# Kernel optimization log

Hardware: AMD Instinct MI355X
Metric: run time of the kernel (lower is better)

## Reference

```python
import jax, jax.numpy as jnp
import numpy as np

B, T, I, H, O = 65536, 28, 28, 64, 10


def setup_inputs() -> dict:
    key = jax.random.key(0)
    ks = jax.random.split(key, 8)
    s = 1.0 / np.sqrt(H)
    return {
        "x": jax.random.normal(ks[0], (B, T, I), dtype=jnp.float32),
        # PyTorch LSTM params: gate order i, f, g, o stacked along first dim
        "W_ih": jax.random.uniform(ks[1], (4 * H, I), minval=-s, maxval=s, dtype=jnp.float32),
        "W_hh": jax.random.uniform(ks[2], (4 * H, H), minval=-s, maxval=s, dtype=jnp.float32),
        "b_ih": jax.random.uniform(ks[3], (4 * H,), minval=-s, maxval=s, dtype=jnp.float32),
        "b_hh": jax.random.uniform(ks[4], (4 * H,), minval=-s, maxval=s, dtype=jnp.float32),
        "W_out": jax.random.uniform(ks[5], (O, H), minval=-s, maxval=s, dtype=jnp.float32),
        "b_out": jax.random.uniform(ks[6], (O,), minval=-s, maxval=s, dtype=jnp.float32),
    }


def _lstm_last_h(x, W_ih, W_hh, b_ih, b_hh):
    # x: [B, T, I]; returns final hidden state h_T: [B, H]
    b = b_ih + b_hh
    # precompute input projections for all timesteps: [T, B, 4H]
    xg = jnp.einsum("bti,gi->tbg", x, W_ih) + b

    def step(carry, xg_t):
        h, c = carry
        gates = xg_t + h @ W_hh.T  # [B, 4H]
        i, f, g, o = jnp.split(gates, 4, axis=-1)
        i = jax.nn.sigmoid(i)
        f = jax.nn.sigmoid(f)
        g = jnp.tanh(g)
        o = jax.nn.sigmoid(o)
        c = f * c + i * g
        h = o * jnp.tanh(c)
        return (h, c), None

    h0 = jnp.zeros((x.shape[0], W_hh.shape[1]), dtype=x.dtype)
    (h, c), _ = jax.lax.scan(step, (h0, h0), xg)
    return h


def reference(x, W_ih, W_hh, b_ih, b_hh, W_out, b_out):
    h = _lstm_last_h(x, W_ih, W_hh, b_ih, b_hh)  # [B, H]
    return h @ W_out.T + b_out  # [B, O]
```

## Files before the change

kernel.cpp:

```cpp
#include <hip/hip_runtime.h>
#include <hip/hip_bf16.h>
#include <stdint.h>
#include <stddef.h>

#define T_STEPS 28
#define I_DIM 28
#define H_DIM 64
#define O_DIM 10
#define BT 64
#define NTHREADS 512

typedef short bf16x8  __attribute__((ext_vector_type(8)));
typedef float f32x4   __attribute__((ext_vector_type(4)));

#define KS (-1.4426950408889634f)
#define KG ( 2.8853900817779268f)

__device__ __forceinline__ short f2bf(float f){
    uint32_t u = __builtin_bit_cast(uint32_t, f);
    u = (u + 0x7fffu + ((u >> 16) & 1u)) >> 16;
    return (short)u;
}
__device__ __forceinline__ float bf2f(short v){
    return __builtin_bit_cast(float, (uint32_t)(uint16_t)v << 16);
}
__device__ __forceinline__ uint32_t pack_bf16x2(float lo, float hi){
    float2 p2; p2.x = lo; p2.y = hi;
    __hip_bfloat162 p = __float22bfloat162_rn(p2);
    uint32_t u;
    __builtin_memcpy(&u, &p, 4);
    return u;
}

#define X_OFF(b)  ((b) * 5120)
#define H_OFF(b)  (10240 + (b) * 9216)
#define SMEM_BYTES (31232 + 48)

__global__ __launch_bounds__(NTHREADS, 4)
void lstm_fused(const float* __restrict__ x,
                const float* __restrict__ W_ih,
                const float* __restrict__ W_hh,
                const float* __restrict__ b_ih,
                const float* __restrict__ b_hh,
                const float* __restrict__ W_out,
                const float* __restrict__ b_out,
                float* __restrict__ out)
{
    __shared__ alignas(16) unsigned char smem[SMEM_BYTES];
    float* wout_t = (float*)(smem + 28672);
    float* bout_s = (float*)(smem + 31232);

    const int tid    = threadIdx.x;
    const int w      = tid >> 6;
    const int jgroup = w & 3;
    const int mgroup = w >> 2;
    const int lane = tid & 63;
    const int col  = lane & 15;
    const int quad = lane >> 4;
    const int jcol = jgroup * 16 + col;
    const int b0   = blockIdx.x * BT;

    bf16x8 wih[4];
    bf16x8 whh[2][4];
    f32x4  bias4[4];
    #pragma unroll
    for (int nt = 0; nt < 4; ++nt){
        const float sc = (nt == 2) ? KG : KS;
        const int n = nt * 64 + jgroup * 16 + col;
        #pragma unroll
        for (int j = 0; j < 8; ++j){
            const int k = quad * 8 + j;
            wih[nt][j] = (k < I_DIM) ? f2bf(sc * W_ih[n * I_DIM + k]) : (short)0;
        }
        #pragma unroll
        for (int s = 0; s < 2; ++s)
            #pragma unroll
            for (int j = 0; j < 8; ++j){
                const int k = s * 32 + quad * 8 + j;
                whh[s][nt][j] = f2bf(sc * W_hh[n * H_DIM + k]);
            }
        const float b = sc * (b_ih[n] + b_hh[n]);
        f32x4 bv; bv[0] = b; bv[1] = b; bv[2] = b; bv[3] = b;
        bias4[nt] = bv;
    }

    for (int idx = tid; idx < H_DIM * O_DIM; idx += NTHREADS){
        const int j = idx / O_DIM;
        const int o = idx - j * O_DIM;
        wout_t[idx] = W_out[o * H_DIM + j];
    }
    if (tid < O_DIM) bout_s[tid] = b_out[tid];

    for (int idx = tid; idx < 64 * 72; idx += NTHREADS)
        ((short*)(smem + H_OFF(0)))[idx] = 0;

    const int row = tid >> 3;
    const int seg = tid & 7;
    const float* pxs = x + (size_t)(b0 + row) * (T_STEPS * I_DIM) + seg * 4;

    float xa[4];
    #pragma unroll
    for (int u = 0; u < 4; ++u)
        xa[u] = (seg * 4 + u < I_DIM) ? pxs[u] : 0.0f;
    pxs += I_DIM;

    float cst[2][4];
    #pragma unroll
    for (int m = 0; m < 2; ++m)
        #pragma unroll
        for (int r = 0; r < 4; ++r) cst[m][r] = 0.0f;

    for (int t = 0; t < T_STEPS; ++t){
        short (*xb)[40] = (short(*)[40])(smem + X_OFF(t & 1));
        {
            uint2 v;
            v.x = pack_bf16x2(xa[0], xa[1]);
            v.y = pack_bf16x2(xa[2], xa[3]);
            *(uint2*)&xb[row][seg * 4] = v;
        }
        __syncthreads();

        if (t < T_STEPS - 1){
            #pragma unroll
            for (int u = 0; u < 4; ++u)
                if (seg * 4 + u < I_DIM) xa[u] = pxs[u];
            pxs += I_DIM;
        }

        const short (*hr)[72] = (const short(*)[72])(smem + H_OFF(t & 1));
        short (*hw)[72]       = (short(*)[72])(smem + H_OFF((t + 1) & 1));

        #pragma unroll
        for (int m = 0; m < 2; ++m){
            const int mt = mgroup * 2 + m;

            f32x4 acc[4];
            {
                bf16x8 a = *(const bf16x8*)&xb[mt * 16 + col][quad * 8];
                #pragma unroll
                for (int nt = 0; nt < 4; ++nt)
                    acc[nt] = __builtin_amdgcn_mfma_f32_16x16x32_bf16(a, wih[nt], bias4[nt], 0, 0, 0);
            }
            #pragma unroll
            for (int s = 0; s < 2; ++s){
                bf16x8 a = *(const bf16x8*)&hr[mt * 16 + col][s * 32 + quad * 8];
                #pragma unroll
                for (int nt = 0; nt < 4; ++nt)
                    acc[nt] = __builtin_amdgcn_mfma_f32_16x16x32_bf16(a, whh[s][nt], acc[nt], 0, 0, 0);
            }

            float hv[4];
            #pragma unroll
            for (int r = 0; r < 4; ++r){
                const float gi = __builtin_amdgcn_rcpf(1.0f + __builtin_amdgcn_exp2f(acc[0][r]));
                const float gf = __builtin_amdgcn_rcpf(1.0f + __builtin_amdgcn_exp2f(acc[1][r]));
                const float rg = __builtin_amdgcn_rcpf(1.0f + __builtin_amdgcn_exp2f(acc[2][r]));
                const float gg = 1.0f - 2.0f * rg;
                const float go = __builtin_amdgcn_rcpf(1.0f + __builtin_amdgcn_exp2f(acc[3][r]));
                const float c_ = gf * cst[m][r] + gi * gg;
                cst[m][r] = c_;
                const float rc = __builtin_amdgcn_rcpf(1.0f + __builtin_amdgcn_exp2f(KG * c_));
                hv[r] = go * (1.0f - 2.0f * rc);
            }
            #pragma unroll
            for (int rp = 0; rp < 2; ++rp){
                uint32_t u = pack_bf16x2(hv[2 * rp], hv[2 * rp + 1]);
                hw[mt * 16 + quad * 4 + 2 * rp    ][jcol] = (short)(u & 0xffffu);
                hw[mt * 16 + quad * 4 + 2 * rp + 1][jcol] = (short)(u >> 16);
            }
        }
    }
    __syncthreads();

    const short (*hfin)[72] = (const short(*)[72])(smem + H_OFF(0));
    for (int idx = tid; idx < BT * O_DIM; idx += NTHREADS){
        const int m = idx / O_DIM;
        const int o = idx - m * O_DIM;
        float s = bout_s[o];
        #pragma unroll 8
        for (int j = 0; j < H_DIM; ++j)
            s += bf2f(hfin[m][j]) * wout_t[j * O_DIM + o];
        out[(size_t)b0 * O_DIM + idx] = s;
    }
}

extern "C" void kernel_launch(void* const* d_in, const int* in_sizes, int n_in,
                              void* d_out, int out_size, void* d_ws, size_t ws_size,
                              hipStream_t stream) {
    const float* x     = (const float*)d_in[0];
    const float* W_ih  = (const float*)d_in[1];
    const float* W_hh  = (const float*)d_in[2];
    const float* b_ih  = (const float*)d_in[3];
    const float* b_hh  = (const float*)d_in[4];
    const float* W_out = (const float*)d_in[5];
    const float* b_out = (const float*)d_in[6];
    float* out = (float*)d_out;

    const int grid = 65536 / BT;
    lstm_fused<<<grid, NTHREADS, 0, stream>>>(x, W_ih, W_hh, b_ih, b_hh, W_out, b_out, out);
}
```

Baseline: 381.1 us.

## Halve block size, share reciprocals across gates, pad hidden stride, unroll time loop

Shrinks each block to 32 batch rows and 256 threads with launch bounds raised to 8 blocks per CU, so more independent blocks can interleave and hide the serial recurrence latency. The gate nonlinearities now pair denominators, computing one reciprocal for two sigmoids (and one for two tanh values), written with packed 2-wide float math to cut transcendental instruction count. The hidden-state LDS row stride goes from 72 to 76 shorts to change bank mapping, and the time loop is unrolled by two. Multiplying two 1+exp terms can overflow to infinity for large gate inputs and lose precision, and the weights are still reloaded per block, so total weight-setup work doubles.

```diff
diff --git a/kernel.cpp b/kernel.cpp
--- a/kernel.cpp
+++ b/kernel.cpp
@@ -7,11 +7,12 @@
 #define I_DIM 28
 #define H_DIM 64
 #define O_DIM 10
-#define BT 64
-#define NTHREADS 512
+#define BT 32
+#define NTHREADS 256
 
 typedef short bf16x8  __attribute__((ext_vector_type(8)));
 typedef float f32x4   __attribute__((ext_vector_type(4)));
+typedef float f32x2   __attribute__((ext_vector_type(2)));
 
 #define KS (-1.4426950408889634f)
 #define KG ( 2.8853900817779268f)
@@ -32,11 +33,12 @@
     return u;
 }
 
-#define X_OFF(b)  ((b) * 5120)
-#define H_OFF(b)  (10240 + (b) * 9216)
-#define SMEM_BYTES (31232 + 48)
-
-__global__ __launch_bounds__(NTHREADS, 4)
+#define X_OFF(b)  ((b) * 2560)
+#define H_OFF(b)  (5120 + (b) * 4864)
+#define H_STRIDE  76
+#define SMEM_BYTES (17408 + 48)
+
+__global__ __launch_bounds__(NTHREADS, 8)
 void lstm_fused(const float* __restrict__ x,
                 const float* __restrict__ W_ih,
                 const float* __restrict__ W_hh,
@@ -47,13 +49,12 @@
                 float* __restrict__ out)
 {
     __shared__ alignas(16) unsigned char smem[SMEM_BYTES];
-    float* wout_t = (float*)(smem + 28672);
-    float* bout_s = (float*)(smem + 31232);
+    float* wout_t = (float*)(smem + 14848);
+    float* bout_s = (float*)(smem + 17408);
 
     const int tid    = threadIdx.x;
     const int w      = tid >> 6;
-    const int jgroup = w & 3;
-    const int mgroup = w >> 2;
+    const int jgroup = w;
     const int lane = tid & 63;
     const int col  = lane & 15;
     const int quad = lane >> 4;
@@ -91,7 +92,7 @@
     }
     if (tid < O_DIM) bout_s[tid] = b_out[tid];
 
-    for (int idx = tid; idx < 64 * 72; idx += NTHREADS)
+    for (int idx = tid; idx < BT * H_STRIDE; idx += NTHREADS)
         ((short*)(smem + H_OFF(0)))[idx] = 0;
 
     const int row = tid >> 3;
@@ -110,6 +111,7 @@
         #pragma unroll
         for (int r = 0; r < 4; ++r) cst[m][r] = 0.0f;
 
+    #pragma unroll 2
     for (int t = 0; t < T_STEPS; ++t){
         short (*xb)[40] = (short(*)[40])(smem + X_OFF(t & 1));
         {
@@ -127,12 +129,12 @@
             pxs += I_DIM;
         }
 
-        const short (*hr)[72] = (const short(*)[72])(smem + H_OFF(t & 1));
-        short (*hw)[72]       = (short(*)[72])(smem + H_OFF((t + 1) & 1));
+        const short (*hr)[H_STRIDE] = (const short(*)[H_STRIDE])(smem + H_OFF(t & 1));
+        short (*hw)[H_STRIDE]       = (short(*)[H_STRIDE])(smem + H_OFF((t + 1) & 1));
 
         #pragma unroll
         for (int m = 0; m < 2; ++m){
-            const int mt = mgroup * 2 + m;
+            const int mt = m;
 
             f32x4 acc[4];
             {
@@ -151,16 +153,35 @@
 
             float hv[4];
             #pragma unroll
-            for (int r = 0; r < 4; ++r){
-                const float gi = __builtin_amdgcn_rcpf(1.0f + __builtin_amdgcn_exp2f(acc[0][r]));
-                const float gf = __builtin_amdgcn_rcpf(1.0f + __builtin_amdgcn_exp2f(acc[1][r]));
-                const float rg = __builtin_amdgcn_rcpf(1.0f + __builtin_amdgcn_exp2f(acc[2][r]));
-                const float gg = 1.0f - 2.0f * rg;
-                const float go = __builtin_amdgcn_rcpf(1.0f + __builtin_amdgcn_exp2f(acc[3][r]));
-                const float c_ = gf * cst[m][r] + gi * gg;
-                cst[m][r] = c_;
-                const float rc = __builtin_amdgcn_rcpf(1.0f + __builtin_amdgcn_exp2f(KG * c_));
-                hv[r] = go * (1.0f - 2.0f * rc);
+            for (int p = 0; p < 2; ++p){
+                const int r0 = 2 * p, r1 = 2 * p + 1;
+                f32x2 EA, EB, EG, EO;
+                EA[0] = __builtin_amdgcn_exp2f(acc[0][r0]); EA[1] = __builtin_amdgcn_exp2f(acc[0][r1]);
+                EB[0] = __builtin_amdgcn_exp2f(acc[1][r0]); EB[1] = __builtin_amdgcn_exp2f(acc[1][r1]);
+                EG[0] = __builtin_amdgcn_exp2f(acc[2][r0]); EG[1] = __builtin_amdgcn_exp2f(acc[2][r1]);
+                EO[0] = __builtin_amdgcn_exp2f(acc[3][r0]); EO[1] = __builtin_amdgcn_exp2f(acc[3][r1]);
+                const f32x2 one = {1.0f, 1.0f};
+                const f32x2 DA = one + EA, DB = one + EB, DG = one + EG, DO = one + EO;
+                const f32x2 pAB = DA * DB, pGO = DG * DO;
+                f32x2 R1, R2;
+                R1[0] = __builtin_amdgcn_rcpf(pAB[0]); R1[1] = __builtin_amdgcn_rcpf(pAB[1]);
+                R2[0] = __builtin_amdgcn_rcpf(pGO[0]); R2[1] = __builtin_amdgcn_rcpf(pGO[1]);
+                const f32x2 iv = R1 * DB;
+                const f32x2 fv = R1 * DA;
+                const f32x2 ov = R2 * DG;
+                const f32x2 gv = one - 2.0f * (R2 * DO);
+                const f32x2 cold = {cst[m][r0], cst[m][r1]};
+                const f32x2 cnew = fv * cold + iv * gv;
+                cst[m][r0] = cnew[0]; cst[m][r1] = cnew[1];
+                f32x2 E5;
+                E5[0] = __builtin_amdgcn_exp2f(KG * cnew[0]);
+                E5[1] = __builtin_amdgcn_exp2f(KG * cnew[1]);
+                const f32x2 D5 = one + E5;
+                const float R5 = __builtin_amdgcn_rcpf(D5[0] * D5[1]);
+                const f32x2 sw = {D5[1], D5[0]};
+                const f32x2 th = one - (2.0f * R5) * sw;
+                const f32x2 hv2 = ov * th;
+                hv[r0] = hv2[0]; hv[r1] = hv2[1];
             }
             #pragma unroll
             for (int rp = 0; rp < 2; ++rp){
@@ -172,7 +193,7 @@
     }
     __syncthreads();
 
-    const short (*hfin)[72] = (const short(*)[72])(smem + H_OFF(0));
+    const short (*hfin)[H_STRIDE] = (const short(*)[H_STRIDE])(smem + H_OFF(0));
     for (int idx = tid; idx < BT * O_DIM; idx += NTHREADS){
         const int m = idx / O_DIM;
         const int o = idx - m * O_DIM;
```

After: 1.330 ms. 249% more time.
